# Optimization experiments

Hardware: AMD Instinct MI355X
Metric: run time of the kernel (lower is better)

## Reference

```python
import jax, jax.numpy as jnp
import numpy as np

F1 = 2   # attention 'time' dim after reshape
F2 = 10  # number of heads
DIN = 2 * F1  # = 4, in/out features of every Linear


def setup_inputs() -> dict:
    key = jax.random.key(0)
    kx, kk, kq, kv = jax.random.split(key, 4)
    B = 1024
    # forward constraints: x is (B, 2B, 2)
    x = jax.random.normal(kx, (B, 2 * B, 2), dtype=jnp.float32)
    # torch Linear default init: U(-1/sqrt(fan_in), 1/sqrt(fan_in)), fan_in=4
    s = 1.0 / np.sqrt(DIN)
    Wk = jax.random.uniform(kk, (F2, DIN, DIN), minval=-s, maxval=s, dtype=jnp.float32)
    Wq = jax.random.uniform(kq, (F2, DIN, DIN), minval=-s, maxval=s, dtype=jnp.float32)
    Wv = jax.random.uniform(kv, (F2, DIN, DIN), minval=-s, maxval=s, dtype=jnp.float32)
    return {"x": x, "Wk": Wk, "Wq": Wq, "Wv": Wv}


def reference(x, Wk, Wq, Wv):
    B, H, T = x.shape          # H = 2B, T = 2 (enforced by the torch views)
    f2 = Wk.shape[0]
    # idy.view(B, -1): flatten each (H, T)=(2B,2) slice row-major into (B, 4)
    xr = x.reshape(B, B, DIN)                       # (B, B, 4)
    # Linear (no bias): y = x @ W.T, batched over the f2 heads; then
    # .view(f1, H): flatten (B,4) row-major -> (2, 2B)
    K = jnp.einsum('bnf,igf->bing', xr, Wk).reshape(B, f2, F1, H)
    Q = jnp.einsum('bnf,igf->bing', xr, Wq).reshape(B, f2, F1, H)
    V = jnp.einsum('bnf,igf->bing', xr, Wv).reshape(B, f2, F1, H)
    # q @ k^T over the H-sized feature dim -> (B, f2, 2, 2)
    scores = jnp.einsum('bitd,bisd->bits', Q, K)
    mask = jnp.tril(jnp.ones((F1, F1), dtype=bool))[:T, :T]
    scores = jnp.where(mask, scores, -jnp.inf)
    wei = jax.nn.softmax(scores, axis=-1)           # (B, f2, 2, 2)
    # (wei @ v).sum(-1, keepdim) per head, concatenated over heads -> (B, 2, f2)
    y = jnp.einsum('bits,bisd->bit', wei, V)        # (B, f2, 2)
    return jnp.transpose(y, (0, 2, 1))              # (B, 2, f2)
```

## Files before the change

### kernel.cpp

```cpp
#include <hip/hip_runtime.h>


#define NB 1024
#define NHEAD 10

__global__ __launch_bounds__(256) void head_kernel(
    const float* __restrict__ x,
    const float* __restrict__ Wk,
    const float* __restrict__ Wq,
    const float* __restrict__ Wv,
    float* __restrict__ out)
{
    const int b = blockIdx.x;
    const int tid = threadIdx.x;
    const float4* x4 = (const float4*)x + (size_t)b * 1024;

    float acc[40];
    #pragma unroll
    for (int k = 0; k < 40; ++k) acc[k] = 0.f;

    #pragma unroll
    for (int p = 0; p < 2; ++p) {
        const int n = tid + p * 256;
        const float4 a0 = x4[n];
        const float4 a1 = x4[512 + n];
        const float v0[4] = {a0.x, a0.y, a0.z, a0.w};
        const float v1[4] = {a1.x, a1.y, a1.z, a1.w};
        #pragma unroll
        for (int f = 0; f < 4; ++f) {
            acc[32 + f] += v0[f];
            acc[36 + f] += v1[f];
            #pragma unroll
            for (int fp = 0; fp < 4; ++fp) {
                acc[f * 4 + fp]      += v1[f] * v0[fp];
                acc[16 + f * 4 + fp] += v1[f] * v1[fp];
            }
        }
    }

    #pragma unroll
    for (int k = 0; k < 40; ++k) {
        float v = acc[k];
        #pragma unroll
        for (int off = 32; off > 0; off >>= 1)
            v += __shfl_down(v, off, 64);
        acc[k] = v;
    }

    __shared__ float red[4][40];
    __shared__ float fin[40];
    const int wave = tid >> 6;
    const int lane = tid & 63;
    if (lane == 0) {
        #pragma unroll
        for (int k = 0; k < 40; ++k) red[wave][k] = acc[k];
    }
    __syncthreads();
    if (tid < 40)
        fin[tid] = red[0][tid] + red[1][tid] + red[2][tid] + red[3][tid];
    __syncthreads();

    if (tid < NHEAD) {
        const int i = tid;
        const float* wq = Wq + i * 16;
        const float* wk = Wk + i * 16;
        const float* wv = Wv + i * 16;

        float sc10 = 0.f, sc11 = 0.f;
        #pragma unroll
        for (int g = 0; g < 4; ++g) {
            #pragma unroll
            for (int f = 0; f < 4; ++f) {
                float a10 = 0.f, a11 = 0.f;
                #pragma unroll
                for (int fp = 0; fp < 4; ++fp) {
                    a10 += fin[f * 4 + fp]      * wk[g * 4 + fp];
                    a11 += fin[16 + f * 4 + fp] * wk[g * 4 + fp];
                }
                sc10 += wq[g * 4 + f] * a10;
                sc11 += wq[g * 4 + f] * a11;
            }
        }

        float wvf[4];
        #pragma unroll
        for (int f = 0; f < 4; ++f)
            wvf[f] = wv[f] + wv[4 + f] + wv[8 + f] + wv[12 + f];

        float vs0 = 0.f, vs1 = 0.f;
        #pragma unroll
        for (int f = 0; f < 4; ++f) {
            vs0 += fin[32 + f] * wvf[f];
            vs1 += fin[36 + f] * wvf[f];
        }

        const float m  = fmaxf(sc10, sc11);
        const float e0 = __expf(sc10 - m);
        const float e1 = __expf(sc11 - m);
        const float inv = 1.f / (e0 + e1);

        out[b * 20 + i]      = vs0;
        out[b * 20 + 10 + i] = (e0 * vs0 + e1 * vs1) * inv;
    }
}

extern "C" void kernel_launch(void* const* d_in, const int* in_sizes, int n_in,
                              void* d_out, int out_size, void* d_ws, size_t ws_size,
                              hipStream_t stream)
{
    const float* x  = (const float*)d_in[0];
    const float* Wk = (const float*)d_in[1];
    const float* Wq = (const float*)d_in[2];
    const float* Wv = (const float*)d_in[3];
    float* out = (float*)d_out;
    head_kernel<<<NB, 256, 0, stream>>>(x, Wk, Wq, Wv, out);
}
```

Baseline: 76.76 us.

## Use one wave per batch row with symmetric Gram and xor-shuffle reduction

Each block shrinks from 256 threads to a single 64-lane wave. Every lane loads 8 float4 pairs up front, and the whole reduction happens with xor shuffles, so the shared-memory staging and both __syncthreads are gone. The v1·v1 Gram matrix is symmetric, so only its upper triangle (10 entries) is accumulated, dropping the accumulator count from 40 to 34. Weights are prefetched as float4 before the reduction. Fewer threads per row means more per-lane serial work and register pressure, which can reduce the latency hiding available for the memory-bound load of x.

```diff
diff --git a/kernel.cpp b/kernel.cpp
--- a/kernel.cpp
+++ b/kernel.cpp
@@ -2,9 +2,12 @@
 
 
 #define NB 1024
-#define NHEAD 10
 
-__global__ __launch_bounds__(256) void head_kernel(
+__device__ __forceinline__ int TRI(int f, int fp) {
+    return f * (7 - f) / 2 + fp;
+}
+
+__global__ __launch_bounds__(64) void head_kernel(
     const float* __restrict__ x,
     const float* __restrict__ Wk,
     const float* __restrict__ Wq,
@@ -12,73 +15,78 @@
     float* __restrict__ out)
 {
     const int b = blockIdx.x;
-    const int tid = threadIdx.x;
+    const int lane = threadIdx.x;
     const float4* x4 = (const float4*)x + (size_t)b * 1024;
 
-    float acc[40];
+    float4 A0[8], A1[8];
     #pragma unroll
-    for (int k = 0; k < 40; ++k) acc[k] = 0.f;
+    for (int p = 0; p < 8; ++p) {
+        A0[p] = x4[lane + p * 64];
+        A1[p] = x4[512 + lane + p * 64];
+    }
+
+    const int hi = lane < 10 ? lane : 0;
+    float4 wq4[4], wk4[4], wv4[4];
+    {
+        const float4* q = (const float4*)(Wq + hi * 16);
+        const float4* k = (const float4*)(Wk + hi * 16);
+        const float4* v = (const float4*)(Wv + hi * 16);
+        #pragma unroll
+        for (int g = 0; g < 4; ++g) { wq4[g] = q[g]; wk4[g] = k[g]; wv4[g] = v[g]; }
+    }
+
+    float acc[34];
+    #pragma unroll
+    for (int k = 0; k < 34; ++k) acc[k] = 0.f;
 
     #pragma unroll
-    for (int p = 0; p < 2; ++p) {
-        const int n = tid + p * 256;
-        const float4 a0 = x4[n];
-        const float4 a1 = x4[512 + n];
-        const float v0[4] = {a0.x, a0.y, a0.z, a0.w};
-        const float v1[4] = {a1.x, a1.y, a1.z, a1.w};
+    for (int p = 0; p < 8; ++p) {
+        const float v0[4] = {A0[p].x, A0[p].y, A0[p].z, A0[p].w};
+        const float v1[4] = {A1[p].x, A1[p].y, A1[p].z, A1[p].w};
         #pragma unroll
         for (int f = 0; f < 4; ++f) {
-            acc[32 + f] += v0[f];
-            acc[36 + f] += v1[f];
+            acc[26 + f] += v0[f];
+            acc[30 + f] += v1[f];
             #pragma unroll
-            for (int fp = 0; fp < 4; ++fp) {
-                acc[f * 4 + fp]      += v1[f] * v0[fp];
-                acc[16 + f * 4 + fp] += v1[f] * v1[fp];
-            }
+            for (int fp = 0; fp < 4; ++fp)
+                acc[f * 4 + fp] += v1[f] * v0[fp];
+            #pragma unroll
+            for (int fp = f; fp < 4; ++fp)
+                acc[16 + TRI(f, fp)] += v1[f] * v1[fp];
         }
     }
 
     #pragma unroll
-    for (int k = 0; k < 40; ++k) {
+    for (int k = 0; k < 34; ++k) {
         float v = acc[k];
         #pragma unroll
-        for (int off = 32; off > 0; off >>= 1)
-            v += __shfl_down(v, off, 64);
+        for (int off = 1; off < 64; off <<= 1)
+            v += __shfl_xor(v, off, 64);
         acc[k] = v;
     }
 
-    __shared__ float red[4][40];
-    __shared__ float fin[40];
-    const int wave = tid >> 6;
-    const int lane = tid & 63;
-    if (lane == 0) {
+    if (lane < 10) {
+        float wq[16], wk[16], wv[16];
         #pragma unroll
-        for (int k = 0; k < 40; ++k) red[wave][k] = acc[k];
-    }
-    __syncthreads();
-    if (tid < 40)
-        fin[tid] = red[0][tid] + red[1][tid] + red[2][tid] + red[3][tid];
-    __syncthreads();
-
-    if (tid < NHEAD) {
-        const int i = tid;
-        const float* wq = Wq + i * 16;
-        const float* wk = Wk + i * 16;
-        const float* wv = Wv + i * 16;
+        for (int g = 0; g < 4; ++g) {
+            wq[g*4+0] = wq4[g].x; wq[g*4+1] = wq4[g].y; wq[g*4+2] = wq4[g].z; wq[g*4+3] = wq4[g].w;
+            wk[g*4+0] = wk4[g].x; wk[g*4+1] = wk4[g].y; wk[g*4+2] = wk4[g].z; wk[g*4+3] = wk4[g].w;
+            wv[g*4+0] = wv4[g].x; wv[g*4+1] = wv4[g].y; wv[g*4+2] = wv4[g].z; wv[g*4+3] = wv4[g].w;
+        }
 
         float sc10 = 0.f, sc11 = 0.f;
         #pragma unroll
-        for (int g = 0; g < 4; ++g) {
+        for (int f = 0; f < 4; ++f) {
             #pragma unroll
-            for (int f = 0; f < 4; ++f) {
-                float a10 = 0.f, a11 = 0.f;
+            for (int fp = 0; fp < 4; ++fp) {
+                float qk = 0.f;
                 #pragma unroll
-                for (int fp = 0; fp < 4; ++fp) {
-                    a10 += fin[f * 4 + fp]      * wk[g * 4 + fp];
-                    a11 += fin[16 + f * 4 + fp] * wk[g * 4 + fp];
-                }
-                sc10 += wq[g * 4 + f] * a10;
-                sc11 += wq[g * 4 + f] * a11;
+                for (int g = 0; g < 4; ++g)
+                    qk += wq[g * 4 + f] * wk[g * 4 + fp];
+                const int lo = f < fp ? f : fp;
+                const int hgh = f < fp ? fp : f;
+                sc10 += qk * acc[f * 4 + fp];
+                sc11 += qk * acc[16 + TRI(lo, hgh)];
             }
         }
 
@@ -90,17 +98,17 @@
         float vs0 = 0.f, vs1 = 0.f;
         #pragma unroll
         for (int f = 0; f < 4; ++f) {
-            vs0 += fin[32 + f] * wvf[f];
-            vs1 += fin[36 + f] * wvf[f];
+            vs0 += acc[26 + f] * wvf[f];
+            vs1 += acc[30 + f] * wvf[f];
         }
 
         const float m  = fmaxf(sc10, sc11);
         const float e0 = __expf(sc10 - m);
         const float e1 = __expf(sc11 - m);
-        const float inv = 1.f / (e0 + e1);
+        const float r  = 1.f / (e0 + e1);
 
-        out[b * 20 + i]      = vs0;
-        out[b * 20 + 10 + i] = (e0 * vs0 + e1 * vs1) * inv;
+        out[b * 20 + lane]      = vs0;
+        out[b * 20 + 10 + lane] = (e0 * vs0 + e1 * vs1) * r;
     }
 }
 
@@ -113,5 +121,5 @@
     const float* Wq = (const float*)d_in[2];
     const float* Wv = (const float*)d_in[3];
     float* out = (float*)d_out;
-    head_kernel<<<NB, 256, 0, stream>>>(x, Wk, Wq, Wv, out);
+    head_kernel<<<NB, 64, 0, stream>>>(x, Wk, Wq, Wv, out);
 }
```

New measurement: 69.60 us. 9.3% less time.
